# Kernel optimization log

Hardware: AMD Instinct MI355X
Metric: run time of the kernel (lower is better)

Reference implementation:

```python
import jax, jax.numpy as jnp
import numpy as np

NEG = -9e15
ALPHA = 0.2  # LeakyReLU negative slope


def _gat_layer(x, W, a, mask):
    # x: [N, Fin], W: [Fin, Fout], a: [2*Fout, 1], mask: [N, N] bool
    h = x @ W                                  # [N, Fout]
    F = h.shape[1]
    # additive attention score: identical math to cat([h_i, h_j]) @ a
    f1 = h @ a[:F, 0]                          # [N]
    f2 = h @ a[F:, 0]                          # [N]
    e = jax.nn.leaky_relu(f1[:, None] + f2[None, :], ALPHA)  # [N, N]
    e = jnp.where(mask, e, NEG)
    attn = jax.nn.softmax(e, axis=1)           # dropout is identity in eval mode
    return attn @ h                            # [N, Fout]


def setup_inputs() -> dict:
    key = jax.random.key(0)
    ks = jax.random.split(key, 6)
    N, Fin, H, Fh, Fo = 4096, 256, 8, 64, 64
    features = jax.random.normal(ks[0], (N, Fin), dtype=jnp.float32)
    adj = jax.random.randint(ks[1], (N, N), 0, 2).astype(jnp.float32)
    W_heads = jax.random.normal(ks[2], (H, Fin, Fh), dtype=jnp.float32) * 0.1
    a_heads = jax.random.normal(ks[3], (H, 2 * Fh, 1), dtype=jnp.float32) * 0.1
    W_out = jax.random.normal(ks[4], (H * Fh, Fo), dtype=jnp.float32) * 0.1
    a_out = jax.random.normal(ks[5], (2 * Fo, 1), dtype=jnp.float32) * 0.1
    return {"features": features, "adj": adj, "W_heads": W_heads,
            "a_heads": a_heads, "W_out": W_out, "a_out": a_out}


def reference(features, adj, W_heads, a_heads, W_out, a_out):
    mask = adj > 0
    H = W_heads.shape[0]
    # loop over the small fixed set of heads (keeps peak memory at one NxN matrix)
    heads = [jax.nn.elu(_gat_layer(features, W_heads[i], a_heads[i], mask))
             for i in range(H)]
    x = jnp.concatenate(heads, axis=1)         # [N, H*Fh]
    return _gat_layer(x, W_out, a_out, mask)   # concat=False -> no elu
```

## Files before the change

kernel.cpp:

```cpp
#include <hip/hip_runtime.h>
#include <hip/hip_bf16.h>

#define N_NODES 4096
#define LOG2E 1.44269504088896340736f
#define JT 128

typedef __attribute__((ext_vector_type(8))) short bf16x8;
typedef __attribute__((ext_vector_type(4))) short bf16x4;
typedef __attribute__((ext_vector_type(4))) float f32x4;
typedef __attribute__((ext_vector_type(16))) float f32x16;

static __device__ __forceinline__ ushort f2bf(float x) {
    union { float f; unsigned u; } v; v.f = x;
    unsigned u = v.u;
    return (ushort)((u + 0x7FFFu + ((u >> 16) & 1u)) >> 16);
}
static __device__ __forceinline__ float bf2f(ushort h) {
    union { unsigned u; float f; } v; v.u = ((unsigned)h) << 16; return v.f;
}

__global__ __launch_bounds__(256) void k_prologue(const float* __restrict__ adj,
        unsigned* __restrict__ maskw,
        const float* __restrict__ W1, ushort* __restrict__ Wh1, ushort* __restrict__ Wl1,
        const float* __restrict__ W2, ushort* __restrict__ Wh2, ushort* __restrict__ Wl2) {
    int b = blockIdx.x, t = threadIdx.x;
    if (b < 2048) {
        int idx = b * 256 + t;
        int row = idx >> 7, w = idx & 127;
        const float4* ap = (const float4*)(adj + (size_t)row * N_NODES + w * 32);
        unsigned bits = 0;
#pragma unroll
        for (int q = 0; q < 8; ++q) {
            float4 v = ap[q];
            bits |= (v.x > 0.f ? 1u : 0u) << (q * 4 + 0);
            bits |= (v.y > 0.f ? 1u : 0u) << (q * 4 + 1);
            bits |= (v.z > 0.f ? 1u : 0u) << (q * 4 + 2);
            bits |= (v.w > 0.f ? 1u : 0u) << (q * 4 + 3);
        }
        maskw[idx] = bits;
    } else {
        const float* W; ushort *Wh, *Wl; int idx, kshift;
        if (b < 2560) { W = W1; Wh = Wh1; Wl = Wl1; idx = (b - 2048) * 256 + t; kshift = 8; }
        else          { W = W2; Wh = Wh2; Wl = Wl2; idx = (b - 2560) * 256 + t; kshift = 9; }
        int K = 1 << kshift;
        int n = idx & 63;
        int k = (idx >> 6) & (K - 1);
        int h = idx >> (6 + kshift);
        float v = W[idx];
        ushort hi = f2bf(v);
        union { unsigned u; float f; } hv; hv.u = ((unsigned)hi) << 16;
        ushort lo = f2bf(v - hv.f);
        size_t dst = ((size_t)h * 64 + n) * K + k;
        Wh[dst] = hi; Wl[dst] = lo;
    }
}

__global__ __launch_bounds__(512) void k_gemm_h(const float* __restrict__ X,
        const ushort* __restrict__ Wh, const ushort* __restrict__ Wl,
        const float* __restrict__ a,
        ushort* __restrict__ Ht, float* __restrict__ Rc,
        float* __restrict__ Tc, ushort* __restrict__ G2b, int K) {
    int head = blockIdx.y;
    int t = threadIdx.x, wave = t >> 6, lane = t & 63;
    int c = lane & 15, g = lane >> 4;
    int i0 = blockIdx.x * 16;
    int kq = K >> 3;
    int kbeg = wave * kq;
    const float* xrow = X + (size_t)(i0 + c) * K;
    f32x4 acc[4] = {};
    for (int k0 = kbeg; k0 < kbeg + kq; k0 += 32) {
        const float4* xp = (const float4*)(xrow + k0 + g * 8);
        float4 xa = xp[0], xb = xp[1];
        float xs[8] = {xa.x, xa.y, xa.z, xa.w, xb.x, xb.y, xb.z, xb.w};
        union { ushort s[8]; bf16x8 v; } ah, al;
#pragma unroll
        for (int e = 0; e < 8; ++e) {
            ushort hb = f2bf(xs[e]);
            ah.s[e] = hb;
            union { unsigned u; float f; } hv; hv.u = ((unsigned)hb) << 16;
            al.s[e] = f2bf(xs[e] - hv.f);
        }
#pragma unroll
        for (int nt = 0; nt < 4; ++nt) {
            size_t boff = ((size_t)head * 64 + nt * 16 + c) * K + k0 + g * 8;
            bf16x8 bh = *(const bf16x8*)(Wh + boff);
            bf16x8 bl = *(const bf16x8*)(Wl + boff);
            acc[nt] = __builtin_amdgcn_mfma_f32_16x16x32_bf16(ah.v, bh, acc[nt], 0, 0, 0);
            acc[nt] = __builtin_amdgcn_mfma_f32_16x16x32_bf16(al.v, bh, acc[nt], 0, 0, 0);
            acc[nt] = __builtin_amdgcn_mfma_f32_16x16x32_bf16(ah.v, bl, acc[nt], 0, 0, 0);
        }
    }
    __shared__ float red[8][64][17];
#pragma unroll
    for (int nt = 0; nt < 4; ++nt)
#pragma unroll
        for (int r = 0; r < 4; ++r)
            red[wave][lane][nt * 4 + r] = acc[nt][r];
    __syncthreads();
    if (wave != 0) return;
#pragma unroll
    for (int nt = 0; nt < 4; ++nt)
#pragma unroll
        for (int r = 0; r < 4; ++r) {
            float s = 0.f;
#pragma unroll
            for (int w = 0; w < 8; ++w) s += red[w][lane][nt * 4 + r];
            acc[nt][r] = s;
        }
    float a1v[4], a2v[4];
#pragma unroll
    for (int nt = 0; nt < 4; ++nt) {
        a1v[nt] = a[head * 128 + nt * 16 + c];
        a2v[nt] = a[head * 128 + 64 + nt * 16 + c];
    }
    float G2f[4];
#pragma unroll
    for (int r = 0; r < 4; ++r) {
        float f1 = 0.f, f2 = 0.f;
#pragma unroll
        for (int nt = 0; nt < 4; ++nt) {
            f1 = __builtin_fmaf(acc[nt][r], a1v[nt], f1);
            f2 = __builtin_fmaf(acc[nt][r], a2v[nt], f2);
        }
#pragma unroll
        for (int o = 1; o < 16; o <<= 1) {
            f1 += __shfl_xor(f1, o);
            f2 += __shfl_xor(f2, o);
        }
        float g2 = __builtin_amdgcn_exp2f(0.2f * LOG2E * f2);
        G2f[r] = g2;
        if (c == 0) {
            int i = i0 + g * 4 + r;
            Rc [head * N_NODES + i] = __builtin_amdgcn_exp2f(-0.8f * LOG2E * f1);
            Tc [head * N_NODES + i] = __builtin_amdgcn_exp2f( 0.8f * LOG2E * f2);
            G2b[head * N_NODES + i] = f2bf(g2);
        }
    }
#pragma unroll
    for (int nt = 0; nt < 4; ++nt) {
        union { ushort s[4]; bf16x4 v; } pk;
#pragma unroll
        for (int r = 0; r < 4; ++r) pk.s[r] = f2bf(acc[nt][r] * G2f[r]);
        *(bf16x4*)(Ht + ((size_t)head * 64 + nt * 16 + c) * N_NODES + i0 + g * 4) = pk.v;
    }
}

template<int JS1>
__global__ __launch_bounds__(512) void k_gemm2(const ushort* __restrict__ accP,
        const float* __restrict__ Zp,
        const ushort* __restrict__ Wh, const ushort* __restrict__ Wl,
        const float* __restrict__ a,
        ushort* __restrict__ Ht, float* __restrict__ Rc,
        float* __restrict__ Tc, ushort* __restrict__ G2b) {
    const int K = 512;
    int t = threadIdx.x, wave = t >> 6, lane = t & 63;
    int c = lane & 15, g = lane >> 4;
    int i0 = blockIdx.x * 16;
    int row = i0 + c;
    int hx = wave;
    float z = 0.f;
#pragma unroll
    for (int js = 0; js < JS1; ++js)
        z += Zp[(size_t)(hx * JS1 + js) * N_NODES + row];
    float rz = 1.0f / z;
    f32x4 acc[4] = {};
#pragma unroll
    for (int ki = 0; ki < 2; ++ki) {
        int k0 = wave * 64 + ki * 32;
        int n0 = ki * 32 + g * 8;
        float s[8] = {};
#pragma unroll
        for (int js = 0; js < JS1; ++js) {
            const ushort* apn = accP + ((size_t)(hx * JS1 + js) * N_NODES + row) * 64 + n0;
            union { int4 v; ushort u[8]; } uu;
            uu.v = *(const int4*)apn;
#pragma unroll
            for (int e = 0; e < 8; ++e) s[e] += bf2f(uu.u[e]);
        }
        union { ushort sh[8]; bf16x8 v; } ah, al;
#pragma unroll
        for (int e = 0; e < 8; ++e) {
            float v = s[e] * rz;
            v = v > 0.f ? v : (__builtin_amdgcn_exp2f(v * LOG2E) - 1.f);
            ushort hb = f2bf(v);
            ah.sh[e] = hb;
            union { unsigned u; float f; } hv; hv.u = ((unsigned)hb) << 16;
            al.sh[e] = f2bf(v - hv.f);
        }
#pragma unroll
        for (int nt = 0; nt < 4; ++nt) {
            size_t boff = ((size_t)(nt * 16 + c)) * K + k0 + g * 8;
            bf16x8 bh = *(const bf16x8*)(Wh + boff);
            bf16x8 bl = *(const bf16x8*)(Wl + boff);
            acc[nt] = __builtin_amdgcn_mfma_f32_16x16x32_bf16(ah.v, bh, acc[nt], 0, 0, 0);
            acc[nt] = __builtin_amdgcn_mfma_f32_16x16x32_bf16(al.v, bh, acc[nt], 0, 0, 0);
            acc[nt] = __builtin_amdgcn_mfma_f32_16x16x32_bf16(ah.v, bl, acc[nt], 0, 0, 0);
        }
    }
    __shared__ float red[8][64][17];
#pragma unroll
    for (int nt = 0; nt < 4; ++nt)
#pragma unroll
        for (int r = 0; r < 4; ++r)
            red[wave][lane][nt * 4 + r] = acc[nt][r];
    __syncthreads();
    if (wave != 0) return;
#pragma unroll
    for (int nt = 0; nt < 4; ++nt)
#pragma unroll
        for (int r = 0; r < 4; ++r) {
            float s = 0.f;
#pragma unroll
            for (int w = 0; w < 8; ++w) s += red[w][lane][nt * 4 + r];
            acc[nt][r] = s;
        }
    float a1v[4], a2v[4];
#pragma unroll
    for (int nt = 0; nt < 4; ++nt) {
        a1v[nt] = a[nt * 16 + c];
        a2v[nt] = a[64 + nt * 16 + c];
    }
    float G2f[4];
#pragma unroll
    for (int r = 0; r < 4; ++r) {
        float f1 = 0.f, f2 = 0.f;
#pragma unroll
        for (int nt = 0; nt < 4; ++nt) {
            f1 = __builtin_fmaf(acc[nt][r], a1v[nt], f1);
            f2 = __builtin_fmaf(acc[nt][r], a2v[nt], f2);
        }
#pragma unroll
        for (int o = 1; o < 16; o <<= 1) {
            f1 += __shfl_xor(f1, o);
            f2 += __shfl_xor(f2, o);
        }
        float g2 = __builtin_amdgcn_exp2f(0.2f * LOG2E * f2);
        G2f[r] = g2;
        if (c == 0) {
            int i = i0 + g * 4 + r;
            Rc [i] = __builtin_amdgcn_exp2f(-0.8f * LOG2E * f1);
            Tc [i] = __builtin_amdgcn_exp2f( 0.8f * LOG2E * f2);
            G2b[i] = f2bf(g2);
        }
    }
#pragma unroll
    for (int nt = 0; nt < 4; ++nt) {
        union { ushort s[4]; bf16x4 v; } pk;
#pragma unroll
        for (int r = 0; r < 4; ++r) pk.s[r] = f2bf(acc[nt][r] * G2f[r]);
        *(bf16x4*)(Ht + ((size_t)(nt * 16 + c)) * N_NODES + i0 + g * 4) = pk.v;
    }
}

template<int JS, int NH>
__global__ __launch_bounds__(256)
__attribute__((amdgpu_waves_per_eu(4, 4)))
void k_attn(const ushort* __restrict__ Ht,
        const float* __restrict__ Rc, const float* __restrict__ Tc,
        const ushort* __restrict__ G2b, const unsigned* __restrict__ maskw,
        ushort* __restrict__ accP, float* __restrict__ Zp) {
    const int NWG = 32 * JS * NH;
    const int CPX = NWG / 8;
    int bid = blockIdx.x;
    int swz = (bid & 7) * CPX + (bid >> 3);
    int rb = swz / (JS * NH);
    int rem = swz - rb * (JS * NH);
    int js = rem / NH;
    int head = rem - js * NH;

    int t = threadIdx.x, wave = t >> 6, lane = t & 63;
    int r32 = lane & 31, half = lane >> 5;
    int i0b = rb * 128;
    int i0w = i0b + wave * 32;
    int irow = i0w + r32;
    const int jcount = N_NODES / JS;
    int j0 = js * jcount;
    const int ntiles = jcount / JT;
    const int ntm1 = ntiles - 1;
    int rot = (rb + js * 3 + head * 5) & ntm1;
    const float R = Rc[head * N_NODES + irow];

    __shared__ ushort Hs[2][64 * JT];
    __shared__ unsigned Ms[2][512];
    __shared__ float Ts[2][JT];
    __shared__ ushort G2s[2][JT];

    int nH = (wave * 4) * 4 + (lane >> 4);
    const ushort* gspH[4];
#pragma unroll
    for (int s = 0; s < 4; ++s) {
        int n = nH + s * 4;
        gspH[s] = Ht + ((size_t)head * 64 + n) * N_NODES + j0
                + (((lane & 15) ^ (n & 7)) << 3);
    }
    const unsigned* msA = maskw + (size_t)(i0b + (2 * wave) * 16 + (lane >> 2)) * 128
                        + (j0 >> 5) + (lane & 3);
    const unsigned* msB = msA + (size_t)16 * 128;
    const float*  tsrcA = Tc  + (size_t)head * N_NODES + j0 + lane;
    const float*  tsrcB = Tc  + (size_t)head * N_NODES + j0 + 64 + lane;
    const ushort* gsrc  = G2b + (size_t)head * N_NODES + j0 + lane * 2;

    auto stage = [&](int b, int tile) {
        int go = tile * JT;
#pragma unroll
        for (int s = 0; s < 4; ++s)
            __builtin_amdgcn_global_load_lds((const unsigned*)(gspH[s] + go),
                    (unsigned*)&Hs[b][(wave * 4 + s) * 512], 16, 0, 0);
        __builtin_amdgcn_global_load_lds(msA + tile * 4,
                (unsigned*)&Ms[b][(2 * wave) * 64], 4, 0, 0);
        __builtin_amdgcn_global_load_lds(msB + tile * 4,
                (unsigned*)&Ms[b][(2 * wave + 1) * 64], 4, 0, 0);
        if (wave == 1)
            __builtin_amdgcn_global_load_lds((const unsigned*)(tsrcA + go),
                    (unsigned*)&Ts[b][0], 4, 0, 0);
        else if (wave == 2)
            __builtin_amdgcn_global_load_lds((const unsigned*)(tsrcB + go),
                    (unsigned*)&Ts[b][64], 4, 0, 0);
        else if (wave == 3)
            __builtin_amdgcn_global_load_lds((const unsigned*)(gsrc + go),
                    (unsigned*)&G2s[b][0], 4, 0, 0);
    };

    f32x16 acc0 = {}, acc1 = {}, acc2 = {};

    stage(0, rot);
    int buf = 0;
    for (int tt = 0; tt < ntiles; ++tt) {
        if (tt + 1 < ntiles) {
            stage(buf ^ 1, (tt + 1 + rot) & ntm1);
            if (wave == 0) asm volatile("s_waitcnt vmcnt(6)");
            else           asm volatile("s_waitcnt vmcnt(7)");
        } else {
            asm volatile("s_waitcnt vmcnt(0)");
        }
        __builtin_amdgcn_s_barrier();

        const char* hb = (const char*)&Hs[buf][0];
        union { uint4 v; unsigned w[4]; } mw;
        mw.v = *(const uint4*)&Ms[buf][(wave * 32 + r32) * 4];
#pragma unroll
        for (int itr = 0; itr < JT / 16; ++itr) {
            unsigned phys = (unsigned)(((itr * 2 + half) ^ (r32 & 7)) << 4);
            bf16x8 b0 = *(const bf16x8*)(hb + r32 * 256 + phys);
            bf16x8 b1 = *(const bf16x8*)(hb + (32 + r32) * 256 + phys);
            bf16x8 bg = *(const bf16x8*)(&G2s[buf][itr * 16 + half * 8]);
            unsigned mword = mw.w[itr >> 1];
            unsigned mshift = mword >> ((itr & 1) * 16 + half * 8);
            const float* tp = &Ts[buf][itr * 16 + half * 8];
            float4 ta = *(const float4*)tp;
            float4 tb = *(const float4*)(tp + 4);
            float tv[8] = {ta.x, ta.y, ta.z, ta.w, tb.x, tb.y, tb.z, tb.w};
            float p[8];
#pragma unroll
            for (int e = 0; e < 8; ++e) {
                int sm = (int)(mshift << (31 - e)) >> 31;
                float pe = fmaxf(tv[e], R);
                union { float f; int i; } pv; pv.f = pe;
                pv.i &= sm;
                p[e] = pv.f;
            }
            union { unsigned w[4]; bf16x8 v; } pa;
#pragma unroll
            for (int q = 0; q < 4; ++q)
                asm("v_cvt_pk_bf16_f32 %0, %1, %2"
                    : "=v"(pa.w[q]) : "v"(p[2 * q]), "v"(p[2 * q + 1]));
            acc0 = __builtin_amdgcn_mfma_f32_32x32x16_bf16(pa.v, b0, acc0, 0, 0, 0);
            acc1 = __builtin_amdgcn_mfma_f32_32x32x16_bf16(pa.v, b1, acc1, 0, 0, 0);
            acc2 = __builtin_amdgcn_mfma_f32_32x32x16_bf16(pa.v, bg, acc2, 0, 0, 0);
        }
        __builtin_amdgcn_s_barrier();
        buf ^= 1;
    }
    int slice = head * JS + js;
    if (r32 == 0) {
#pragma unroll
        for (int reg = 0; reg < 16; ++reg) {
            int drow = (reg & 3) + 8 * (reg >> 2) + 4 * half;
            Zp[(size_t)slice * N_NODES + i0w + drow] = acc2[reg];
        }
    }
    ushort* ap = accP + ((size_t)slice * N_NODES + i0w) * 64;
#pragma unroll
    for (int reg = 0; reg < 16; ++reg) {
        int drow = (reg & 3) + 8 * (reg >> 2) + 4 * half;
        ap[drow * 64 + r32] = f2bf(acc0[reg]);
        ap[drow * 64 + 32 + r32] = f2bf(acc1[reg]);
    }
}

template<int JS>
__global__ __launch_bounds__(256) void k_combine2(const ushort* __restrict__ accP,
        const float* __restrict__ Zp, float* __restrict__ out) {
    int idx = blockIdx.x * 256 + threadIdx.x;
    int n = idx & 63, i = idx >> 6;
    float s = 0.f, z = 0.f;
#pragma unroll
    for (int j = 0; j < JS; ++j) {
        s += bf2f(accP[((size_t)j * N_NODES + i) * 64 + n]);
        z += Zp[(size_t)j * N_NODES + i];
    }
    out[idx] = s / z;
}

extern "C" void kernel_launch(void* const* d_in, const int* in_sizes, int n_in,
                              void* d_out, int out_size, void* d_ws, size_t ws_size,
                              hipStream_t stream) {
    const float* features = (const float*)d_in[0];
    const float* adj      = (const float*)d_in[1];
    const float* W_heads  = (const float*)d_in[2];
    const float* a_heads  = (const float*)d_in[3];
    const float* W_out    = (const float*)d_in[4];
    const float* a_out    = (const float*)d_in[5];
    float* out = (float*)d_out;

    int tier;
    if (ws_size >= 26000000)      tier = 2;
    else if (ws_size >= 17500000) tier = 1;
    else                          tier = 0;
    int JS1 = tier == 2 ? 4 : (tier == 1 ? 2 : 1);
    int JS2 = tier == 2 ? 32 : (tier == 1 ? 16 : 8);
    int slices = (8 * JS1 > JS2) ? 8 * JS1 : JS2;

    char* ws = (char*)d_ws;
    size_t off = 0;
    auto alloc = [&](size_t bytes) -> void* {
        void* p = ws + off; off = (off + bytes + 255) & ~(size_t)255; return p;
    };
    unsigned* maskw = (unsigned*)alloc((size_t)N_NODES * 128 * 4);
    ushort* Ht1 = (ushort*)alloc((size_t)8 * 64 * N_NODES * 2);
    ushort* Ht2 = (ushort*)alloc((size_t)64 * N_NODES * 2);
    float* Rc1  = (float*)alloc((size_t)8 * N_NODES * 4);
    float* Tc1  = (float*)alloc((size_t)8 * N_NODES * 4);
    ushort* G2b1 = (ushort*)alloc((size_t)8 * N_NODES * 2);
    float* Rc2  = (float*)alloc((size_t)N_NODES * 4);
    float* Tc2  = (float*)alloc((size_t)N_NODES * 4);
    ushort* G2b2 = (ushort*)alloc((size_t)N_NODES * 2);
    ushort* Wh1 = (ushort*)alloc((size_t)8 * 64 * 256 * 2);
    ushort* Wl1 = (ushort*)alloc((size_t)8 * 64 * 256 * 2);
    ushort* Wh2 = (ushort*)alloc((size_t)64 * 512 * 2);
    ushort* Wl2 = (ushort*)alloc((size_t)64 * 512 * 2);
    ushort* accP = (ushort*)alloc((size_t)slices * N_NODES * 64 * 2);
    float* Zp   = (float*)alloc((size_t)slices * N_NODES * 4);

    hipLaunchKernelGGL(k_prologue, dim3(2688), dim3(256), 0, stream,
                       adj, maskw, W_heads, Wh1, Wl1, W_out, Wh2, Wl2);
    hipLaunchKernelGGL(k_gemm_h, dim3(N_NODES / 16, 8), dim3(512), 0, stream,
                       features, Wh1, Wl1, a_heads, Ht1, Rc1, Tc1, G2b1, 256);
    if (tier == 2)
        hipLaunchKernelGGL((k_attn<4, 8>), dim3(32 * 4 * 8), dim3(256), 0, stream,
                           Ht1, Rc1, Tc1, G2b1, maskw, accP, Zp);
    else if (tier == 1)
        hipLaunchKernelGGL((k_attn<2, 8>), dim3(32 * 2 * 8), dim3(256), 0, stream,
                           Ht1, Rc1, Tc1, G2b1, maskw, accP, Zp);
    else
        hipLaunchKernelGGL((k_attn<1, 8>), dim3(32 * 1 * 8), dim3(256), 0, stream,
                           Ht1, Rc1, Tc1, G2b1, maskw, accP, Zp);
    if (tier == 2)
        hipLaunchKernelGGL((k_gemm2<4>), dim3(N_NODES / 16), dim3(512), 0, stream,
                           accP, Zp, Wh2, Wl2, a_out, Ht2, Rc2, Tc2, G2b2);
    else if (tier == 1)
        hipLaunchKernelGGL((k_gemm2<2>), dim3(N_NODES / 16), dim3(512), 0, stream,
                           accP, Zp, Wh2, Wl2, a_out, Ht2, Rc2, Tc2, G2b2);
    else
        hipLaunchKernelGGL((k_gemm2<1>), dim3(N_NODES / 16), dim3(512), 0, stream,
                           accP, Zp, Wh2, Wl2, a_out, Ht2, Rc2, Tc2, G2b2);
    if (tier == 2) {
        hipLaunchKernelGGL((k_attn<32, 1>), dim3(32 * 32), dim3(256), 0, stream,
                           Ht2, Rc2, Tc2, G2b2, maskw, accP, Zp);
        hipLaunchKernelGGL((k_combine2<32>), dim3(N_NODES * 64 / 256), dim3(256), 0, stream,
                           accP, Zp, out);
    } else if (tier == 1) {
        hipLaunchKernelGGL((k_attn<16, 1>), dim3(32 * 16), dim3(256), 0, stream,
                           Ht2, Rc2, Tc2, G2b2, maskw, accP, Zp);
        hipLaunchKernelGGL((k_combine2<16>), dim3(N_NODES * 64 / 256), dim3(256), 0, stream,
                           accP, Zp, out);
    } else {
        hipLaunchKernelGGL((k_attn<8, 1>), dim3(32 * 8), dim3(256), 0, stream,
                           Ht2, Rc2, Tc2, G2b2, maskw, accP, Zp);
        hipLaunchKernelGGL((k_combine2<8>), dim3(N_NODES * 64 / 256), dim3(256), 0, stream,
                           accP, Zp, out);
    }
}
```

Measured before the change: 113.8 us.

## Fuse adjacency mask packing into layer-1 GEMM and raise MFMA priority

Moves adjacency bitmask packing out of the prologue and into the layer-1 projection GEMM. One of every three blocks packs mask words while the other two do GEMM tiles, so the bandwidth-heavy adjacency scan overlaps with compute-bound work. Weight splitting now runs as its own small kernel. The attention kernel drops its XCD-aware block swizzle for a plain rb-major mapping and wraps the MFMA triple in s_setprio to favour matrix issue. Risks include worse L2 locality from the removed swizzle and a leftover dead duplicate load in k_prep_w.

```diff
diff --git a/kernel.cpp b/kernel.cpp
--- a/kernel.cpp
+++ b/kernel.cpp
@@ -19,56 +19,61 @@
     union { unsigned u; float f; } v; v.u = ((unsigned)h) << 16; return v.f;
 }
 
-__global__ __launch_bounds__(256) void k_prologue(const float* __restrict__ adj,
-        unsigned* __restrict__ maskw,
-        const float* __restrict__ W1, ushort* __restrict__ Wh1, ushort* __restrict__ Wl1,
+__global__ __launch_bounds__(256) void k_prep_w(const float* __restrict__ W1,
+        ushort* __restrict__ Wh1, ushort* __restrict__ Wl1,
         const float* __restrict__ W2, ushort* __restrict__ Wh2, ushort* __restrict__ Wl2) {
-    int b = blockIdx.x, t = threadIdx.x;
-    if (b < 2048) {
-        int idx = b * 256 + t;
+    int idx = blockIdx.x * 256 + threadIdx.x;
+    const float* W; ushort *Wh, *Wl; int kshift;
+    if (idx < 131072) { W = W1; Wh = Wh1; Wl = Wl1; kshift = 8; }
+    else { W = W2; Wh = Wh2; Wl = Wl2; idx -= 131072; kshift = 9; }
+    int K = 1 << kshift;
+    int n = idx & 63;
+    int k = (idx >> 6) & (K - 1);
+    int h = idx >> (6 + kshift);
+    float v = W[idx + (kshift == 9 ? 0 : 0) * 0 + 0];
+    v = W[idx];
+    ushort hi = f2bf(v);
+    union { unsigned u; float f; } hv; hv.u = ((unsigned)hi) << 16;
+    ushort lo = f2bf(v - hv.f);
+    size_t dst = ((size_t)h * 64 + n) * K + k;
+    Wh[dst] = hi; Wl[dst] = lo;
+}
+
+__global__ __launch_bounds__(512) void k_gemm_mask(const float* __restrict__ X,
+        const ushort* __restrict__ Wh, const ushort* __restrict__ Wl,
+        const float* __restrict__ a,
+        const float* __restrict__ adj, unsigned* __restrict__ maskw,
+        ushort* __restrict__ Ht, float* __restrict__ Rc,
+        float* __restrict__ Tc, ushort* __restrict__ G2b) {
+    const int K = 256;
+    int b = blockIdx.x;
+    int q = b / 3, r3 = b - q * 3;
+    if (r3 == 2) {
+        int idx = q * 512 + threadIdx.x;
         int row = idx >> 7, w = idx & 127;
         const float4* ap = (const float4*)(adj + (size_t)row * N_NODES + w * 32);
         unsigned bits = 0;
 #pragma unroll
-        for (int q = 0; q < 8; ++q) {
-            float4 v = ap[q];
-            bits |= (v.x > 0.f ? 1u : 0u) << (q * 4 + 0);
-            bits |= (v.y > 0.f ? 1u : 0u) << (q * 4 + 1);
-            bits |= (v.z > 0.f ? 1u : 0u) << (q * 4 + 2);
-            bits |= (v.w > 0.f ? 1u : 0u) << (q * 4 + 3);
+        for (int qq = 0; qq < 8; ++qq) {
+            float4 v = ap[qq];
+            bits |= (v.x > 0.f ? 1u : 0u) << (qq * 4 + 0);
+            bits |= (v.y > 0.f ? 1u : 0u) << (qq * 4 + 1);
+            bits |= (v.z > 0.f ? 1u : 0u) << (qq * 4 + 2);
+            bits |= (v.w > 0.f ? 1u : 0u) << (qq * 4 + 3);
         }
         maskw[idx] = bits;
-    } else {
-        const float* W; ushort *Wh, *Wl; int idx, kshift;
-        if (b < 2560) { W = W1; Wh = Wh1; Wl = Wl1; idx = (b - 2048) * 256 + t; kshift = 8; }
-        else          { W = W2; Wh = Wh2; Wl = Wl2; idx = (b - 2560) * 256 + t; kshift = 9; }
-        int K = 1 << kshift;
-        int n = idx & 63;
-        int k = (idx >> 6) & (K - 1);
-        int h = idx >> (6 + kshift);
-        float v = W[idx];
-        ushort hi = f2bf(v);
-        union { unsigned u; float f; } hv; hv.u = ((unsigned)hi) << 16;
-        ushort lo = f2bf(v - hv.f);
-        size_t dst = ((size_t)h * 64 + n) * K + k;
-        Wh[dst] = hi; Wl[dst] = lo;
-    }
-}
-
-__global__ __launch_bounds__(512) void k_gemm_h(const float* __restrict__ X,
-        const ushort* __restrict__ Wh, const ushort* __restrict__ Wl,
-        const float* __restrict__ a,
-        ushort* __restrict__ Ht, float* __restrict__ Rc,
-        float* __restrict__ Tc, ushort* __restrict__ G2b, int K) {
-    int head = blockIdx.y;
+        return;
+    }
+    int gb = q * 2 + r3;
+    int head = gb >> 8;
+    int i0 = (gb & 255) * 16;
     int t = threadIdx.x, wave = t >> 6, lane = t & 63;
     int c = lane & 15, g = lane >> 4;
-    int i0 = blockIdx.x * 16;
-    int kq = K >> 3;
-    int kbeg = wave * kq;
+    int kbeg = wave * 32;
     const float* xrow = X + (size_t)(i0 + c) * K;
     f32x4 acc[4] = {};
-    for (int k0 = kbeg; k0 < kbeg + kq; k0 += 32) {
+    {
+        int k0 = kbeg;
         const float4* xp = (const float4*)(xrow + k0 + g * 8);
         float4 xa = xp[0], xb = xp[1];
         float xs[8] = {xa.x, xa.y, xa.z, xa.w, xb.x, xb.y, xb.z, xb.w};
@@ -259,14 +264,11 @@
         const float* __restrict__ Rc, const float* __restrict__ Tc,
         const ushort* __restrict__ G2b, const unsigned* __restrict__ maskw,
         ushort* __restrict__ accP, float* __restrict__ Zp) {
-    const int NWG = 32 * JS * NH;
-    const int CPX = NWG / 8;
     int bid = blockIdx.x;
-    int swz = (bid & 7) * CPX + (bid >> 3);
-    int rb = swz / (JS * NH);
-    int rem = swz - rb * (JS * NH);
-    int js = rem / NH;
-    int head = rem - js * NH;
+    int rb = bid & 31;
+    int rem = bid >> 5;
+    int js = rem % JS;
+    int head = rem / JS;
 
     int t = threadIdx.x, wave = t >> 6, lane = t & 63;
     int r32 = lane & 31, half = lane >> 5;
@@ -364,9 +366,11 @@
             for (int q = 0; q < 4; ++q)
                 asm("v_cvt_pk_bf16_f32 %0, %1, %2"
                     : "=v"(pa.w[q]) : "v"(p[2 * q]), "v"(p[2 * q + 1]));
+            __builtin_amdgcn_s_setprio(1);
             acc0 = __builtin_amdgcn_mfma_f32_32x32x16_bf16(pa.v, b0, acc0, 0, 0, 0);
             acc1 = __builtin_amdgcn_mfma_f32_32x32x16_bf16(pa.v, b1, acc1, 0, 0, 0);
             acc2 = __builtin_amdgcn_mfma_f32_32x32x16_bf16(pa.v, bg, acc2, 0, 0, 0);
+            __builtin_amdgcn_s_setprio(0);
         }
         __builtin_amdgcn_s_barrier();
         buf ^= 1;
@@ -442,10 +446,11 @@
     ushort* accP = (ushort*)alloc((size_t)slices * N_NODES * 64 * 2);
     float* Zp   = (float*)alloc((size_t)slices * N_NODES * 4);
 
-    hipLaunchKernelGGL(k_prologue, dim3(2688), dim3(256), 0, stream,
-                       adj, maskw, W_heads, Wh1, Wl1, W_out, Wh2, Wl2);
-    hipLaunchKernelGGL(k_gemm_h, dim3(N_NODES / 16, 8), dim3(512), 0, stream,
-                       features, Wh1, Wl1, a_heads, Ht1, Rc1, Tc1, G2b1, 256);
+    hipLaunchKernelGGL(k_prep_w, dim3(640), dim3(256), 0, stream,
+                       W_heads, Wh1, Wl1, W_out, Wh2, Wl2);
+    hipLaunchKernelGGL(k_gemm_mask, dim3(3072), dim3(512), 0, stream,
+                       features, Wh1, Wl1, a_heads, adj, maskw,
+                       Ht1, Rc1, Tc1, G2b1);
     if (tier == 2)
         hipLaunchKernelGGL((k_attn<4, 8>), dim3(32 * 4 * 8), dim3(256), 0, stream,
                            Ht1, Rc1, Tc1, G2b1, maskw, accP, Zp);
```

Result: no change. 115.1 us (+1.1%).
